# Optimization experiments

Hardware: AMD Instinct MI355X
Metric: run time of the kernel (lower is better)

## Reference

```python
import jax, jax.numpy as jnp
import numpy as np

B, S, D, H = 16, 1024, 768, 12
DH = D // H


def setup_inputs() -> dict:
    key = jax.random.key(0)
    ks = jax.random.split(key, 9)
    s = 0.02
    return {
        "sequences": jax.random.normal(ks[0], (B, S, D), dtype=jnp.float32),
        # per-head Linear weights stored as [H, in, out] (i.e. torch W.T per head)
        "Wq": jax.random.normal(ks[1], (H, DH, DH), dtype=jnp.float32) * s,
        "bq": jax.random.normal(ks[2], (H, DH), dtype=jnp.float32) * s,
        "Wk": jax.random.normal(ks[3], (H, DH, DH), dtype=jnp.float32) * s,
        "bk": jax.random.normal(ks[4], (H, DH), dtype=jnp.float32) * s,
        "Wv": jax.random.normal(ks[5], (H, DH, DH), dtype=jnp.float32) * s,
        "bv": jax.random.normal(ks[6], (H, DH), dtype=jnp.float32) * s,
        # final Linear: W_last is [in, out] (torch W.T), b_last [out]
        "W_last": jax.random.normal(ks[7], (D, D), dtype=jnp.float32) * s,
        "b_last": jax.random.normal(ks[8], (D,), dtype=jnp.float32) * s,
    }


def reference(sequences, Wq, bq, Wk, bk, Wv, bv, W_last, b_last):
    # split token dim into heads: [B, S, H, DH] (head h sees slice h*DH:(h+1)*DH)
    x = sequences.reshape(B, S, H, DH)
    q = jnp.einsum("bshd,hde->bshe", x, Wq) + bq  # [B,S,H,DH]
    k = jnp.einsum("bshd,hde->bshe", x, Wk) + bk
    v = jnp.einsum("bshd,hde->bshe", x, Wv) + bv
    scale = 1.0 / np.sqrt(DH).astype(np.float32)
    scores = jnp.einsum("bqhd,bkhd->bhqk", q, k) * scale  # [B,H,S,S]
    attn = jax.nn.softmax(scores, axis=-1)
    out = jnp.einsum("bhqk,bkhd->bqhd", attn, v)  # [B,S,H,DH]
    out = out.reshape(B, S, D)
    return out @ W_last + b_last
```

## Files before the change

kernel.cpp:

```cpp
#include <hip/hip_runtime.h>


#define NB 16
#define NS 1024
#define ND 768
#define NH 12
#define NDH 64
#define LDH 72
#define QSCALE 0.18033688f

typedef _Float16 half8 __attribute__((ext_vector_type(8)));
typedef _Float16 half4 __attribute__((ext_vector_type(4)));
typedef float floatx4 __attribute__((ext_vector_type(4)));

__global__ __launch_bounds__(256) void wqkv_prep(
    const float* __restrict__ Wq, const float* __restrict__ Wk,
    const float* __restrict__ Wv, _Float16* __restrict__ Wt)
{
    __shared__ float sh[64][65];
    const int m = blockIdx.x, h = blockIdx.y, tid = threadIdx.x;
    const float* Wsrc = (m == 0 ? Wq : (m == 1 ? Wk : Wv)) + h * 4096;
    const float scale = (m == 0) ? QSCALE : 1.0f;
    #pragma unroll
    for (int p = 0; p < 4; ++p) {
        int fi = tid + p * 256, r = fi >> 4, c4 = (fi & 15) * 4;
        *(float4*)&sh[r][c4] = *(const float4*)(Wsrc + r * 64 + c4);
    }
    __syncthreads();
    const int dout = tid >> 2, ks = (tid & 3) * 16;
    union { _Float16 h_[8]; float4 f; } pk;
    #pragma unroll
    for (int g = 0; g < 2; ++g) {
        #pragma unroll
        for (int j = 0; j < 8; ++j) pk.h_[j] = (_Float16)(sh[ks + 8 * g + j][dout] * scale);
        *(float4*)(Wt + ((long)((m * 12 + h) * 64 + dout)) * 64 + ks + 8 * g) = pk.f;
    }
}

__global__ __launch_bounds__(256) void wt_kernel(
    const float* __restrict__ Wl, _Float16* __restrict__ Wt)
{
    __shared__ float sh[64][65];
    const int tid = threadIdx.x;
    const int k0 = blockIdx.x * 64, n0 = blockIdx.y * 64;
    #pragma unroll
    for (int p = 0; p < 4; ++p) {
        int fi = tid + p * 256, kk = fi >> 4, c4 = (fi & 15) * 4;
        *(float4*)&sh[kk][c4] = *(const float4*)(Wl + (long)(k0 + kk) * ND + n0 + c4);
    }
    __syncthreads();
    const int nn = tid >> 2, ks = (tid & 3) * 16;
    union { _Float16 h_[8]; float4 f; } pk;
    #pragma unroll
    for (int g = 0; g < 2; ++g) {
        #pragma unroll
        for (int j = 0; j < 8; ++j) pk.h_[j] = (_Float16)sh[ks + 8 * g + j][nn];
        *(float4*)(Wt + (long)(n0 + nn) * ND + k0 + ks + 8 * g) = pk.f;
    }
}

__global__ __launch_bounds__(256) void qkv_kernel(
    const float* __restrict__ seq, const _Float16* __restrict__ Wt,
    const float* __restrict__ bq, const float* __restrict__ bk, const float* __restrict__ bv,
    _Float16* __restrict__ Qo, _Float16* __restrict__ Ko, _Float16* __restrict__ Vo)
{
    __shared__ _Float16 Xs[128][LDH];
    __shared__ _Float16 Ws[3][64][LDH];
    const int tid = threadIdx.x, w = tid >> 6, lane = tid & 63;
    const int quad = lane >> 4, lx = lane & 15;
    const int bx = blockIdx.x, h = blockIdx.y;
    const long tok0 = (long)bx * 128;
    const int b = bx >> 3, s0 = (bx & 7) * 128;
    const long hb = (long)b * NH + h;

    #pragma unroll
    for (int p = 0; p < 4; ++p) {
        int fi = tid + p * 256, r = fi >> 3, c8 = (fi & 7) * 8;
        const float* src = seq + (tok0 + r) * ND + h * NDH + c8;
        float4 f0 = *(const float4*)src, f1 = *(const float4*)(src + 4);
        union { _Float16 h_[8]; float4 f; } pk;
        pk.h_[0] = (_Float16)f0.x; pk.h_[1] = (_Float16)f0.y;
        pk.h_[2] = (_Float16)f0.z; pk.h_[3] = (_Float16)f0.w;
        pk.h_[4] = (_Float16)f1.x; pk.h_[5] = (_Float16)f1.y;
        pk.h_[6] = (_Float16)f1.z; pk.h_[7] = (_Float16)f1.w;
        *(float4*)&Xs[r][c8] = pk.f;
    }
    #pragma unroll
    for (int p = 0; p < 6; ++p) {
        int fi = tid + p * 256, m = fi >> 9, r = (fi >> 3) & 63, c8 = (fi & 7) * 8;
        *(float4*)&Ws[m][r][c8] = *(const float4*)(Wt + ((long)((m * 12 + h) * 64 + r)) * 64 + c8);
    }
    __syncthreads();

    half8 a[2][2];
    #pragma unroll
    for (int mb = 0; mb < 2; ++mb)
        #pragma unroll
        for (int kk = 0; kk < 2; ++kk)
            a[mb][kk] = *(const half8*)&Xs[32 * w + 16 * mb + lx][8 * quad + 32 * kk];

    const float* biases[3] = {bq, bk, bv};
    #pragma unroll
    for (int m = 0; m < 3; ++m) {
        half8 bf[4][2];
        #pragma unroll
        for (int nt = 0; nt < 4; ++nt)
            #pragma unroll
            for (int kk = 0; kk < 2; ++kk)
                bf[nt][kk] = *(const half8*)&Ws[m][16 * nt + lx][8 * quad + 32 * kk];
        floatx4 acc[2][4];
        #pragma unroll
        for (int mb = 0; mb < 2; ++mb)
            #pragma unroll
            for (int nt = 0; nt < 4; ++nt) acc[mb][nt] = (floatx4)0.f;
        #pragma unroll
        for (int kk = 0; kk < 2; ++kk)
            #pragma unroll
            for (int mb = 0; mb < 2; ++mb)
                #pragma unroll
                for (int nt = 0; nt < 4; ++nt)
                    acc[mb][nt] = __builtin_amdgcn_mfma_f32_16x16x32_f16(a[mb][kk], bf[nt][kk], acc[mb][nt], 0, 0, 0);

        const float bsc = (m == 0) ? QSCALE : 1.0f;
        #pragma unroll
        for (int nt = 0; nt < 4; ++nt) {
            const float bvv = biases[m][h * NDH + 16 * nt + lx] * bsc;
            #pragma unroll
            for (int mb = 0; mb < 2; ++mb)
                #pragma unroll
                for (int p = 0; p < 4; ++p) {
                    const int tl = 32 * w + 16 * mb + 4 * quad + p;
                    const _Float16 hv = (_Float16)(acc[mb][nt][p] + bvv);
                    if (m == 0)
                        Qo[(hb * NS + s0 + tl) * NDH + 16 * nt + lx] = hv;
                    else if (m == 1)
                        Ko[(hb * NS + s0 + tl) * NDH + 16 * nt + lx] = hv;
                    else
                        Vo[(hb * NDH + 16 * nt + lx) * NS + s0 + tl] = hv;
                }
        }
    }
}

__global__ __launch_bounds__(256) void attn_kernel(
    const _Float16* __restrict__ Q, const _Float16* __restrict__ K,
    const _Float16* __restrict__ Vt, _Float16* __restrict__ O)
{
    __shared__ _Float16 Qs[128][LDH];
    __shared__ _Float16 Ks[64][LDH];
    __shared__ _Float16 Vs[64][LDH];

    const int tid = threadIdx.x, w = tid >> 6, lane = tid & 63;
    const int quad = lane >> 4, lx = lane & 15;
    const int flat = blockIdx.x;
    const int xcd = flat & 7, rest = flat >> 3;
    const int qb = rest & 7, bhg = rest >> 3;
    const int bh = bhg * 8 + xcd;
    const int bb = bh / NH, h = bh % NH;
    const int q0 = qb * 128;
    const long hb = bh;

    #pragma unroll
    for (int p = 0; p < 4; ++p) {
        int fi = tid + p * 256, r = fi >> 3, c8 = (fi & 7) * 8;
        *(float4*)&Qs[r][c8] = *(const float4*)(Q + (hb * NS + q0 + r) * NDH + c8);
    }
    __syncthreads();

    half8 bq[2][2];
    #pragma unroll
    for (int qb2 = 0; qb2 < 2; ++qb2)
        #pragma unroll
        for (int kk = 0; kk < 2; ++kk)
            bq[qb2][kk] = *(const half8*)&Qs[32 * w + 16 * qb2 + lx][8 * quad + 32 * kk];

    float l_acc[2] = {0.f, 0.f};
    floatx4 o_acc[2][4];
    #pragma unroll
    for (int qb2 = 0; qb2 < 2; ++qb2)
        #pragma unroll
        for (int nt = 0; nt < 4; ++nt) o_acc[qb2][nt] = (floatx4)0.f;

    for (int kt = 0; kt < NS / 64; ++kt) {
        __syncthreads();
        #pragma unroll
        for (int p = 0; p < 2; ++p) {
            int fi = tid + p * 256, r = fi >> 3, c8 = (fi & 7) * 8;
            *(float4*)&Ks[r][c8] = *(const float4*)(K  + (hb * NS + kt * 64 + r) * NDH + c8);
            *(float4*)&Vs[r][c8] = *(const float4*)(Vt + (hb * NDH + r) * NS + kt * 64 + c8);
        }
        __syncthreads();

        half8 ak[4][2];
        #pragma unroll
        for (int jt = 0; jt < 4; ++jt)
            #pragma unroll
            for (int kk = 0; kk < 2; ++kk)
                ak[jt][kk] = *(const half8*)&Ks[16 * jt + lx][8 * quad + 32 * kk];

        half4 af[2][4];
        #pragma unroll
        for (int qb2 = 0; qb2 < 2; ++qb2) {
            #pragma unroll
            for (int jt = 0; jt < 4; ++jt) {
                floatx4 st = (floatx4)0.f;
                st = __builtin_amdgcn_mfma_f32_16x16x32_f16(ak[jt][0], bq[qb2][0], st, 0, 0, 0);
                st = __builtin_amdgcn_mfma_f32_16x16x32_f16(ak[jt][1], bq[qb2][1], st, 0, 0, 0);
                float e0 = __builtin_amdgcn_exp2f(st[0]);
                float e1 = __builtin_amdgcn_exp2f(st[1]);
                float e2 = __builtin_amdgcn_exp2f(st[2]);
                float e3 = __builtin_amdgcn_exp2f(st[3]);
                l_acc[qb2] += (e0 + e1) + (e2 + e3);
                half4 pf;
                pf[0] = (_Float16)e0; pf[1] = (_Float16)e1;
                pf[2] = (_Float16)e2; pf[3] = (_Float16)e3;
                af[qb2][jt] = pf;
            }
        }

        #pragma unroll
        for (int nt = 0; nt < 4; ++nt) {
            half4 vf[4];
            #pragma unroll
            for (int jt = 0; jt < 4; ++jt)
                vf[jt] = *(const half4*)&Vs[16 * nt + lx][16 * jt + 4 * quad];
            #pragma unroll
            for (int qb2 = 0; qb2 < 2; ++qb2)
                #pragma unroll
                for (int jt = 0; jt < 4; ++jt)
                    o_acc[qb2][nt] = __builtin_amdgcn_mfma_f32_16x16x16f16(af[qb2][jt], vf[jt], o_acc[qb2][nt], 0, 0, 0);
        }
    }

    #pragma unroll
    for (int qb2 = 0; qb2 < 2; ++qb2) {
        float l = l_acc[qb2];
        l += __shfl_xor(l, 16);
        l += __shfl_xor(l, 32);
        #pragma unroll
        for (int p = 0; p < 4; ++p) {
            const float inv = 1.f / __shfl(l, 4 * quad + p);
            const long row = (long)bb * NS + q0 + 32 * w + 16 * qb2 + 4 * quad + p;
            #pragma unroll
            for (int nt = 0; nt < 4; ++nt)
                O[row * ND + h * NDH + 16 * nt + lx] = (_Float16)(o_acc[qb2][nt][p] * inv);
        }
    }
}

__global__ __launch_bounds__(256) void out_proj_kernel(
    const _Float16* __restrict__ X, const _Float16* __restrict__ Wt,
    const float* __restrict__ bl, float* __restrict__ out)
{
    __shared__ _Float16 Ah[128][LDH];
    __shared__ _Float16 Bh[128][LDH];

    const int tid = threadIdx.x, w = tid >> 6, lane = tid & 63;
    const int quad = lane >> 4, lx = lane & 15;
    const int wm = (w >> 1) * 64, wn = (w & 1) * 64;
    const long r0 = (long)blockIdx.x * 128;
    const int c0 = blockIdx.y * 128;

    floatx4 acc[4][4];
    #pragma unroll
    for (int mt = 0; mt < 4; ++mt)
        #pragma unroll
        for (int nt = 0; nt < 4; ++nt) acc[mt][nt] = (floatx4)0.f;

    for (int kt = 0; kt < ND / 64; ++kt) {
        __syncthreads();
        #pragma unroll
        for (int p = 0; p < 4; ++p) {
            int fi = tid + p * 256, r = fi >> 3, c8 = (fi & 7) * 8;
            *(float4*)&Ah[r][c8] = *(const float4*)(X  + (r0 + r) * ND + kt * 64 + c8);
            *(float4*)&Bh[r][c8] = *(const float4*)(Wt + (long)(c0 + r) * ND + kt * 64 + c8);
        }
        __syncthreads();

        #pragma unroll
        for (int kk = 0; kk < 2; ++kk) {
            half8 a[4], b[4];
            #pragma unroll
            for (int mt = 0; mt < 4; ++mt)
                a[mt] = *(const half8*)&Ah[wm + 16 * mt + lx][kk * 32 + quad * 8];
            #pragma unroll
            for (int nt = 0; nt < 4; ++nt)
                b[nt] = *(const half8*)&Bh[wn + 16 * nt + lx][kk * 32 + quad * 8];
            #pragma unroll
            for (int mt = 0; mt < 4; ++mt)
                #pragma unroll
                for (int nt = 0; nt < 4; ++nt)
                    acc[mt][nt] = __builtin_amdgcn_mfma_f32_16x16x32_f16(a[mt], b[nt], acc[mt][nt], 0, 0, 0);
        }
    }

    #pragma unroll
    for (int mt = 0; mt < 4; ++mt)
        #pragma unroll
        for (int nt = 0; nt < 4; ++nt) {
            const int col = c0 + wn + 16 * nt + lx;
            const float bv = bl[col];
            #pragma unroll
            for (int p = 0; p < 4; ++p) {
                const long row = r0 + wm + 16 * mt + quad * 4 + p;
                out[row * ND + col] = acc[mt][nt][p] + bv;
            }
        }
}

extern "C" void kernel_launch(void* const* d_in, const int* in_sizes, int n_in,
                              void* d_out, int out_size, void* d_ws, size_t ws_size,
                              hipStream_t stream) {
    const float* seq    = (const float*)d_in[0];
    const float* Wq     = (const float*)d_in[1];
    const float* bq     = (const float*)d_in[2];
    const float* Wk     = (const float*)d_in[3];
    const float* bk     = (const float*)d_in[4];
    const float* Wv     = (const float*)d_in[5];
    const float* bv     = (const float*)d_in[6];
    const float* W_last = (const float*)d_in[7];
    const float* b_last = (const float*)d_in[8];
    float* out = (float*)d_out;

    const long HN = (long)NB * NH * NS * NDH;
    _Float16* qh   = (_Float16*)d_ws;
    _Float16* kh   = qh + HN;
    _Float16* vt   = kh + HN;
    _Float16* xh   = vt + HN;
    _Float16* wtL  = xh + (long)NB * NS * ND;
    _Float16* wtQKV = wtL + (long)ND * ND;

    wqkv_prep<<<dim3(3, NH), 256, 0, stream>>>(Wq, Wk, Wv, wtQKV);
    wt_kernel<<<dim3(ND / 64, ND / 64), 256, 0, stream>>>(W_last, wtL);
    qkv_kernel<<<dim3(NB * NS / 128, NH), 256, 0, stream>>>(seq, wtQKV, bq, bk, bv, qh, kh, vt);
    attn_kernel<<<NB * NH * (NS / 128), 256, 0, stream>>>(qh, kh, vt, xh);
    out_proj_kernel<<<dim3(NB * NS / 128, ND / 128), 256, 0, stream>>>(xh, wtL, b_last, out);
}
```

Baseline: 244.1 us.

## Transpose MFMA operands for vectorized stores and drop Q shared staging

The QKV projection now computes the transposed product (weights as A, tokens as B), so each lane holds four contiguous output features. Q and K can then be stored as half4 vectors, and bias is folded into the accumulator init. V is transposed through shared memory and written with coalesced 16-byte stores. In attention, Q fragments are loaded straight from global memory instead of staged in LDS, the PV MFMA operands are swapped so the output store is half4-vectorized and needs no per-row shuffle, and launch bounds request higher occupancy; this trades extra syncs in the projection and possibly uncoalesced Q loads for fewer scattered 2-byte stores.

```diff
diff --git a/kernel.cpp b/kernel.cpp
--- a/kernel.cpp
+++ b/kernel.cpp
@@ -92,61 +92,79 @@
     }
     __syncthreads();
 
-    half8 a[2][2];
-    #pragma unroll
-    for (int mb = 0; mb < 2; ++mb)
+    half8 xb[2][2];
+    #pragma unroll
+    for (int nt = 0; nt < 2; ++nt)
         #pragma unroll
         for (int kk = 0; kk < 2; ++kk)
-            a[mb][kk] = *(const half8*)&Xs[32 * w + 16 * mb + lx][8 * quad + 32 * kk];
+            xb[nt][kk] = *(const half8*)&Xs[16 * (2 * w + nt) + lx][8 * quad + 32 * kk];
 
     const float* biases[3] = {bq, bk, bv};
     #pragma unroll
     for (int m = 0; m < 3; ++m) {
-        half8 bf[4][2];
-        #pragma unroll
-        for (int nt = 0; nt < 4; ++nt)
+        half8 wa[4][2];
+        #pragma unroll
+        for (int mt = 0; mt < 4; ++mt)
             #pragma unroll
             for (int kk = 0; kk < 2; ++kk)
-                bf[nt][kk] = *(const half8*)&Ws[m][16 * nt + lx][8 * quad + 32 * kk];
-        floatx4 acc[2][4];
-        #pragma unroll
-        for (int mb = 0; mb < 2; ++mb)
-            #pragma unroll
-            for (int nt = 0; nt < 4; ++nt) acc[mb][nt] = (floatx4)0.f;
+                wa[mt][kk] = *(const half8*)&Ws[m][16 * mt + lx][8 * quad + 32 * kk];
+
+        const float bsc = (m == 0) ? QSCALE : 1.0f;
+        floatx4 acc[4][2];
+        #pragma unroll
+        for (int mt = 0; mt < 4; ++mt) {
+            float4 b4 = *(const float4*)&biases[m][h * NDH + 16 * mt + 4 * quad];
+            floatx4 bi; bi[0] = b4.x * bsc; bi[1] = b4.y * bsc; bi[2] = b4.z * bsc; bi[3] = b4.w * bsc;
+            #pragma unroll
+            for (int nt = 0; nt < 2; ++nt) acc[mt][nt] = bi;
+        }
         #pragma unroll
         for (int kk = 0; kk < 2; ++kk)
             #pragma unroll
-            for (int mb = 0; mb < 2; ++mb)
-                #pragma unroll
-                for (int nt = 0; nt < 4; ++nt)
-                    acc[mb][nt] = __builtin_amdgcn_mfma_f32_16x16x32_f16(a[mb][kk], bf[nt][kk], acc[mb][nt], 0, 0, 0);
-
-        const float bsc = (m == 0) ? QSCALE : 1.0f;
-        #pragma unroll
-        for (int nt = 0; nt < 4; ++nt) {
-            const float bvv = biases[m][h * NDH + 16 * nt + lx] * bsc;
-            #pragma unroll
-            for (int mb = 0; mb < 2; ++mb)
-                #pragma unroll
-                for (int p = 0; p < 4; ++p) {
-                    const int tl = 32 * w + 16 * mb + 4 * quad + p;
-                    const _Float16 hv = (_Float16)(acc[mb][nt][p] + bvv);
-                    if (m == 0)
-                        Qo[(hb * NS + s0 + tl) * NDH + 16 * nt + lx] = hv;
-                    else if (m == 1)
-                        Ko[(hb * NS + s0 + tl) * NDH + 16 * nt + lx] = hv;
-                    else
-                        Vo[(hb * NDH + 16 * nt + lx) * NS + s0 + tl] = hv;
+            for (int mt = 0; mt < 4; ++mt)
+                #pragma unroll
+                for (int nt = 0; nt < 2; ++nt)
+                    acc[mt][nt] = __builtin_amdgcn_mfma_f32_16x16x32_f16(wa[mt][kk], xb[nt][kk], acc[mt][nt], 0, 0, 0);
+
+        if (m < 2) {
+            _Float16* Out = (m == 0) ? Qo : Ko;
+            #pragma unroll
+            for (int nt = 0; nt < 2; ++nt) {
+                const long token = s0 + 16 * (2 * w + nt) + lx;
+                #pragma unroll
+                for (int mt = 0; mt < 4; ++mt) {
+                    half4 pk;
+                    #pragma unroll
+                    for (int p = 0; p < 4; ++p) pk[p] = (_Float16)acc[mt][nt][p];
+                    *(half4*)&Out[(hb * NS + token) * NDH + 16 * mt + 4 * quad] = pk;
                 }
-        }
-    }
-}
-
-__global__ __launch_bounds__(256) void attn_kernel(
+            }
+        } else {
+            __syncthreads();
+            _Float16 (*Vb)[136] = (_Float16(*)[136])&Xs[0][0];
+            #pragma unroll
+            for (int nt = 0; nt < 2; ++nt) {
+                const int tok = 16 * (2 * w + nt) + lx;
+                #pragma unroll
+                for (int mt = 0; mt < 4; ++mt)
+                    #pragma unroll
+                    for (int p = 0; p < 4; ++p)
+                        Vb[16 * mt + 4 * quad + p][tok] = (_Float16)acc[mt][nt][p];
+            }
+            __syncthreads();
+            #pragma unroll
+            for (int p = 0; p < 4; ++p) {
+                int fi = tid + p * 256, r = fi >> 4, c8 = (fi & 15) * 8;
+                *(float4*)(Vo + (hb * NDH + r) * NS + s0 + c8) = *(float4*)&Vb[r][c8];
+            }
+        }
+    }
+}
+
+__global__ __launch_bounds__(256, 8) void attn_kernel(
     const _Float16* __restrict__ Q, const _Float16* __restrict__ K,
     const _Float16* __restrict__ Vt, _Float16* __restrict__ O)
 {
-    __shared__ _Float16 Qs[128][LDH];
     __shared__ _Float16 Ks[64][LDH];
     __shared__ _Float16 Vs[64][LDH];
 
@@ -160,19 +178,12 @@
     const int q0 = qb * 128;
     const long hb = bh;
 
-    #pragma unroll
-    for (int p = 0; p < 4; ++p) {
-        int fi = tid + p * 256, r = fi >> 3, c8 = (fi & 7) * 8;
-        *(float4*)&Qs[r][c8] = *(const float4*)(Q + (hb * NS + q0 + r) * NDH + c8);
-    }
-    __syncthreads();
-
     half8 bq[2][2];
     #pragma unroll
     for (int qb2 = 0; qb2 < 2; ++qb2)
         #pragma unroll
         for (int kk = 0; kk < 2; ++kk)
-            bq[qb2][kk] = *(const half8*)&Qs[32 * w + 16 * qb2 + lx][8 * quad + 32 * kk];
+            bq[qb2][kk] = *(const half8*)(Q + (hb * NS + q0 + 32 * w + 16 * qb2 + lx) * NDH + 8 * quad + 32 * kk);
 
     float l_acc[2] = {0.f, 0.f};
     floatx4 o_acc[2][4];
@@ -228,7 +239,7 @@
             for (int qb2 = 0; qb2 < 2; ++qb2)
                 #pragma unroll
                 for (int jt = 0; jt < 4; ++jt)
-                    o_acc[qb2][nt] = __builtin_amdgcn_mfma_f32_16x16x16f16(af[qb2][jt], vf[jt], o_acc[qb2][nt], 0, 0, 0);
+                    o_acc[qb2][nt] = __builtin_amdgcn_mfma_f32_16x16x16f16(vf[jt], af[qb2][jt], o_acc[qb2][nt], 0, 0, 0);
         }
     }
 
@@ -237,13 +248,14 @@
         float l = l_acc[qb2];
         l += __shfl_xor(l, 16);
         l += __shfl_xor(l, 32);
-        #pragma unroll
-        for (int p = 0; p < 4; ++p) {
-            const float inv = 1.f / __shfl(l, 4 * quad + p);
-            const long row = (long)bb * NS + q0 + 32 * w + 16 * qb2 + 4 * quad + p;
-            #pragma unroll
-            for (int nt = 0; nt < 4; ++nt)
-                O[row * ND + h * NDH + 16 * nt + lx] = (_Float16)(o_acc[qb2][nt][p] * inv);
+        const float inv = 1.f / l;
+        const long row = (long)bb * NS + q0 + 32 * w + 16 * qb2 + lx;
+        #pragma unroll
+        for (int nt = 0; nt < 4; ++nt) {
+            half4 pk;
+            #pragma unroll
+            for (int p = 0; p < 4; ++p) pk[p] = (_Float16)(o_acc[qb2][nt][p] * inv);
+            *(half4*)(O + row * ND + h * NDH + 16 * nt + 4 * quad) = pk;
         }
     }
 }
```

Result: slower. 704.9 us (+188.8%).
